# Optimization experiments

Measured on AMD Instinct MI355X. Metric: run time of the kernel, lower is better.

## Reference

```python
import jax, jax.numpy as jnp
import numpy as np

N = 50000
E = 1000000
WIDTH = 64
DEPTH = 4


def setup_inputs() -> dict:
    key = jax.random.key(0)
    ks = jax.random.split(key, 6)
    x = jax.random.normal(ks[0], (N, 5), dtype=jnp.float32)
    edge_index = jax.random.randint(ks[1], (2, E), 0, N, dtype=jnp.int32)
    edge_attr = jax.random.normal(ks[2], (E, 3), dtype=jnp.float32)
    w1 = jax.random.normal(ks[3], (3, WIDTH), dtype=jnp.float32) / jnp.sqrt(3.0)
    b1 = jnp.zeros((WIDTH,), jnp.float32)
    w2 = jax.random.normal(ks[4], (WIDTH, 1), dtype=jnp.float32) / jnp.sqrt(float(WIDTH))
    b2 = jnp.zeros((1,), jnp.float32)
    root = jax.random.normal(ks[5], (1, 1), dtype=jnp.float32)
    bias = jnp.zeros((1,), jnp.float32)
    return dict(x=x, edge_index=edge_index, edge_attr=edge_attr,
                w1=w1, b1=b1, w2=w2, b2=b2, root=root, bias=bias)


def reference(x, edge_index, edge_attr, w1, b1, w2, b2, root, bias):
    # h: scalar node feature, column 2 of data.x -> [N, 1]
    h = x[:, 2:3]
    src, dst = edge_index[0], edge_index[1]  # messages flow src -> dst

    # Per-edge 1x1 weight from the edge MLP (depends only on edge_attr,
    # identical for all depth iterations since the conv is shared).
    w_e = jax.nn.relu(edge_attr @ w1 + b1) @ w2 + b2  # [E, 1]

    # Mean aggregation: precompute in-degree of each target node.
    deg = jax.ops.segment_sum(jnp.ones((E,), jnp.float32), dst, num_segments=N)
    inv_deg = jnp.where(deg > 0, 1.0 / jnp.maximum(deg, 1.0), 0.0)[:, None]  # [N, 1]

    for _ in range(DEPTH):
        msg = h[src] * w_e                                        # gather + per-edge weight, [E, 1]
        agg = jax.ops.segment_sum(msg, dst, num_segments=N) * inv_deg  # scatter-mean, [N, 1]
        h = jax.nn.relu(agg + h @ root + bias)                    # root transform + bias + ReLU
    return h
```

## Files before the change

kernel.cpp:

```cpp
#include <hip/hip_runtime.h>

#define NN 50000
#define NNP 50176
#define NE 1000000
#define NBK 196
#define ESTRIDE 5632
#define EPB4 5120

#define EPB 1024
#define PB 977

__global__ __launch_bounds__(1024)
void place4(const float* __restrict__ x,
            const float* __restrict__ ea,
            const int* __restrict__ src,
            const int* __restrict__ dst,
            const float* __restrict__ w1,
            const float* __restrict__ b1,
            const float* __restrict__ w2,
            const float* __restrict__ b2,
            uint2* __restrict__ es,
            int* __restrict__ ebase,
            float* __restrict__ hA) {
    __shared__ float sw1[192];
    __shared__ float sb1[64];
    __shared__ float sw2[64];
    __shared__ int hist[NBK];
    __shared__ int part[256];
    __shared__ int lexcl[NBK];
    __shared__ uint2 eLDS[EPB4];
    const int t = threadIdx.x;
    const int j = blockIdx.x;
    if (t < 192) sw1[t] = w1[t];
    if (t < 64) { sb1[t] = b1[t]; sw2[t] = w2[t]; }
    if (t < NBK) hist[t] = 0;
    {
        int i = j * 1024 + t;
        if (i < NN) hA[i] = x[5 * i + 2];
    }
    __syncthreads();
    const float bz = b2[0];
    const int e0 = j * EPB4;
    const int myN = (NE - e0 < EPB4) ? (NE - e0) : EPB4;

    float ce[5];
    int dd[5], rr[5], ss[5];
#pragma unroll
    for (int k = 0; k < 5; ++k) {
        int p = k * 1024 + t;
        dd[k] = -1;
        if (p < myN) {
            int e = e0 + p;
            float a0 = ea[3 * e + 0];
            float a1 = ea[3 * e + 1];
            float a2 = ea[3 * e + 2];
            float c0 = bz, c1 = 0.f, c2 = 0.f, c3 = 0.f;
#pragma unroll
            for (int kk = 0; kk < 64; kk += 4) {
                float h0 = fmaf(a0, sw1[kk+0], fmaf(a1, sw1[64+kk+0], fmaf(a2, sw1[128+kk+0], sb1[kk+0])));
                float h1 = fmaf(a0, sw1[kk+1], fmaf(a1, sw1[64+kk+1], fmaf(a2, sw1[128+kk+1], sb1[kk+1])));
                float h2 = fmaf(a0, sw1[kk+2], fmaf(a1, sw1[64+kk+2], fmaf(a2, sw1[128+kk+2], sb1[kk+2])));
                float h3 = fmaf(a0, sw1[kk+3], fmaf(a1, sw1[64+kk+3], fmaf(a2, sw1[128+kk+3], sb1[kk+3])));
                c0 = fmaf(fmaxf(h0, 0.f), sw2[kk+0], c0);
                c1 = fmaf(fmaxf(h1, 0.f), sw2[kk+1], c1);
                c2 = fmaf(fmaxf(h2, 0.f), sw2[kk+2], c2);
                c3 = fmaf(fmaxf(h3, 0.f), sw2[kk+3], c3);
            }
            ce[k] = (c0 + c1) + (c2 + c3);
            ss[k] = src[e];
            int d = dst[e];
            dd[k] = d;
            rr[k] = atomicAdd(&hist[d >> 8], 1);
        }
    }
    __syncthreads();
    int val = 0;
    if (t < 256) { val = (t < NBK) ? hist[t] : 0; part[t] = val; }
    __syncthreads();
    for (int off = 1; off < 256; off <<= 1) {
        int xv = 0, add = 0;
        if (t < 256) { xv = part[t]; if (t >= off) add = part[t - off]; }
        __syncthreads();
        if (t < 256) part[t] = xv + add;
        __syncthreads();
    }
    if (t < NBK) {
        int excl = part[t] - val;
        lexcl[t] = excl;
        ebase[j * NBK + t] = (excl << 16) | val;
    }
    __syncthreads();
#pragma unroll
    for (int k = 0; k < 5; ++k) {
        if (dd[k] >= 0) {
            int d = dd[k];
            int pos = lexcl[d >> 8] + rr[k];
            eLDS[pos] = make_uint2((unsigned)ss[k] | ((unsigned)(d & 255) << 17),
                                   __float_as_uint(ce[k]));
        }
    }
    __syncthreads();
    for (int p = t; p < myN; p += 1024)
        es[e0 + p] = eLDS[p];
}

__global__ __launch_bounds__(1024)
void sortround1(const int* __restrict__ ebase,
                const uint2* __restrict__ es,
                uint2* __restrict__ es2,
                uint2* __restrict__ nodePtr,
                const float* __restrict__ hold,
                float* __restrict__ hnew,
                const float* __restrict__ root,
                const float* __restrict__ bias) {
    __shared__ int cbase[NBK + 1];
    __shared__ int cex[NBK];
    __shared__ int hist[256];
    __shared__ int part[256];
    __shared__ int cur[256];
    __shared__ float lagg[256];
    const int t = threadIdx.x;
    const int b = blockIdx.x;
    if (t < 256) { hist[t] = 0; lagg[t] = 0.f; }
    int c = 0;
    if (t < NBK) {
        int pk = ebase[t * NBK + b];
        cex[t] = pk >> 16;
        c = pk & 0xFFFF;
    }
    if (t < 256) part[t] = (t < NBK) ? c : 0;
    __syncthreads();
    for (int off = 1; off < 256; off <<= 1) {
        int xv = 0, add = 0;
        if (t < 256) { xv = part[t]; if (t >= off) add = part[t - off]; }
        __syncthreads();
        if (t < 256) part[t] = xv + add;
        __syncthreads();
    }
    if (t < NBK) cbase[t] = part[t] - c;
    if (t == 0) cbase[NBK] = part[NBK - 1];
    __syncthreads();
    const int C = cbase[NBK];

    uint2 v[6]; int key[6]; bool m[6];
#pragma unroll
    for (int k = 0; k < 6; ++k) {
        int p = k * 1024 + t;
        m[k] = (p < C);
        if (m[k]) {
            int lo = 0, hi = NBK - 1;
            while (lo < hi) { int mid = (lo + hi + 1) >> 1; if (cbase[mid] <= p) lo = mid; else hi = mid - 1; }
            v[k] = es[lo * EPB4 + cex[lo] + (p - cbase[lo])];
            key[k] = (v[k].x >> 17) & 255;
            atomicAdd(&hist[key[k]], 1);
        }
    }
    __syncthreads();
    int val = 0;
    if (t < 256) { val = hist[t]; part[t] = val; }
    __syncthreads();
    for (int off = 1; off < 256; off <<= 1) {
        int xv = 0, add = 0;
        if (t < 256) { xv = part[t]; if (t >= off) add = part[t - off]; }
        __syncthreads();
        if (t < 256) part[t] = xv + add;
        __syncthreads();
    }
    if (t < 256) {
        int excl = part[t] - val;
        cur[t] = excl;
        int ec = (excl < ESTRIDE) ? excl : ESTRIDE;
        nodePtr[b * 256 + t] = make_uint2((unsigned)(b * ESTRIDE + ec), (unsigned)val);
    }
    __syncthreads();
#pragma unroll
    for (int k = 0; k < 6; ++k) {
        if (m[k]) {
            int pos = atomicAdd(&cur[key[k]], 1);
            if (pos < ESTRIDE) es2[b * ESTRIDE + pos] = v[k];
            atomicAdd(&lagg[key[k]], hold[v[k].x & 0x1FFFF] * __uint_as_float(v[k].y));
        }
    }
    __syncthreads();
    if (t < 256) {
        int node = b * 256 + t;
        if (node < NN) {
            float inv = (val > 0) ? (1.0f / (float)val) : 0.f;
            hnew[node] = fmaxf(fmaf(hold[node], root[0], fmaf(lagg[t], inv, bias[0])), 0.f);
        }
    }
}

__global__ __launch_bounds__(256)
void round_csr(const uint2* __restrict__ nodePtr,
               const uint2* __restrict__ es2,
               const float* __restrict__ hold,
               float* __restrict__ hnew,
               const float* __restrict__ root,
               const float* __restrict__ bias) {
    int g = blockIdx.x * 256 + threadIdx.x;
    int row = g >> 3;
    int sub = g & 7;
    uint2 pk = nodePtr[row];
    int beg = (int)pk.x;
    int len = (int)pk.y;
    float acc = 0.f;
    for (int k = sub; k < len; k += 8) {
        uint2 v = es2[beg + k];
        acc += hold[v.x & 0x1FFFF] * __uint_as_float(v.y);
    }
    acc += __shfl_xor(acc, 1);
    acc += __shfl_xor(acc, 2);
    acc += __shfl_xor(acc, 4);
    if (sub == 0 && row < NN) {
        float inv = (len > 0) ? (1.0f / (float)len) : 0.f;
        hnew[row] = fmaxf(fmaf(hold[row], root[0], fmaf(acc, inv, bias[0])), 0.f);
    }
}

__global__ void bucket_count(const int* __restrict__ dst, int* __restrict__ bcnt,
                             const float* __restrict__ x, float* __restrict__ h) {
    __shared__ int hist[NBK];
    int t = threadIdx.x;
    if (t < NBK) hist[t] = 0;
    __syncthreads();
    int gid = blockIdx.x * 256 + t;
    if (gid < NN) h[gid] = x[5 * gid + 2];
#pragma unroll
    for (int j = 0; j < 4; ++j) {
        int e = blockIdx.x * EPB + j * 256 + t;
        if (e < NE) atomicAdd(&hist[dst[e] >> 8], 1);
    }
    __syncthreads();
    if (t < NBK && hist[t]) atomicAdd(&bcnt[t], hist[t]);
}

__global__ void bucket_scan(const int* __restrict__ bcnt,
                            int* __restrict__ sBeg,
                            int* __restrict__ cursor,
                            int* __restrict__ sLim) {
    __shared__ int part[256];
    int t = threadIdx.x;
    int v = (t < NBK) ? ((bcnt[t] + 1) & ~1) : 0;
    part[t] = v;
    __syncthreads();
    for (int off = 1; off < 256; off <<= 1) {
        int x = part[t];
        int add = (t >= off) ? part[t - off] : 0;
        __syncthreads();
        part[t] = x + add;
        __syncthreads();
    }
    if (t < NBK) {
        int excl = part[t] - v;
        sBeg[t] = excl;
        cursor[t] = excl;
        sLim[t] = 0x7FFFFFFF;
    }
}

__global__ void place_kernel(const float* __restrict__ ea,
                             const int* __restrict__ src,
                             const int* __restrict__ dst,
                             const float* __restrict__ w1,
                             const float* __restrict__ b1,
                             const float* __restrict__ w2,
                             const float* __restrict__ b2,
                             const int* __restrict__ sLim,
                             int* __restrict__ cursor,
                             uint2* __restrict__ es,
                             int dumpbase) {
    __shared__ float sw1[192];
    __shared__ float sb1[64];
    __shared__ float sw2[64];
    __shared__ float sce[EPB];
    __shared__ int hist[NBK];
    __shared__ int hbase[NBK];
    int t = threadIdx.x;
    if (t < 192) sw1[t] = w1[t];
    if (t < 64) { sb1[t] = b1[t]; sw2[t] = w2[t]; }
    if (t < NBK) hist[t] = 0;
    __syncthreads();

    int r[4], dd[4];
#pragma unroll
    for (int j = 0; j < 4; ++j) {
        int e = blockIdx.x * EPB + j * 256 + t;
        dd[j] = -1;
        if (e < NE) {
            float a0 = ea[3 * e + 0];
            float a1 = ea[3 * e + 1];
            float a2 = ea[3 * e + 2];
            float c0 = b2[0], c1 = 0.f, c2 = 0.f, c3 = 0.f;
#pragma unroll
            for (int k = 0; k < 64; k += 4) {
                float h0 = fmaf(a0, sw1[k+0], fmaf(a1, sw1[64+k+0], fmaf(a2, sw1[128+k+0], sb1[k+0])));
                float h1 = fmaf(a0, sw1[k+1], fmaf(a1, sw1[64+k+1], fmaf(a2, sw1[128+k+1], sb1[k+1])));
                float h2 = fmaf(a0, sw1[k+2], fmaf(a1, sw1[64+k+2], fmaf(a2, sw1[128+k+2], sb1[k+2])));
                float h3 = fmaf(a0, sw1[k+3], fmaf(a1, sw1[64+k+3], fmaf(a2, sw1[128+k+3], sb1[k+3])));
                c0 = fmaf(fmaxf(h0, 0.f), sw2[k+0], c0);
                c1 = fmaf(fmaxf(h1, 0.f), sw2[k+1], c1);
                c2 = fmaf(fmaxf(h2, 0.f), sw2[k+2], c2);
                c3 = fmaf(fmaxf(h3, 0.f), sw2[k+3], c3);
            }
            sce[j * 256 + t] = (c0 + c1) + (c2 + c3);
            int d = dst[e];
            dd[j] = d;
            r[j] = atomicAdd(&hist[d >> 8], 1);
        }
    }
    __syncthreads();
    if (t < NBK) { int hv = hist[t]; if (hv) hbase[t] = atomicAdd(&cursor[t], hv); }
    __syncthreads();
#pragma unroll
    for (int j = 0; j < 4; ++j) {
        int e = blockIdx.x * EPB + j * 256 + t;
        if (e < NE) {
            int d = dd[j];
            int b = d >> 8;
            int pos = hbase[b] + r[j];
            if (pos >= sLim[b]) pos = dumpbase + (t & 63);
            unsigned pack = (unsigned)src[e] | ((unsigned)(d & 255) << 17);
            es[pos] = make_uint2(pack, __float_as_uint(sce[j * 256 + t]));
        }
    }
}

template<int FIRST>
__global__ __launch_bounds__(1024)
void round_fused_fb(const int* __restrict__ sBeg,
                    const int* __restrict__ sEnd,
                    const int* __restrict__ sLim,
                    const uint2* __restrict__ es,
                    const float* __restrict__ hold,
                    float* __restrict__ hnew,
                    float* __restrict__ invdeg,
                    const float* __restrict__ root,
                    const float* __restrict__ bias) {
    __shared__ float lagg[256];
    __shared__ int ldeg[256];
    int t = threadIdx.x;
    int b = blockIdx.x;
    if (t < 256) { lagg[t] = 0.f; if (FIRST) ldeg[t] = 0; }
    __syncthreads();
    int s0 = sBeg[b];
    int s1 = sEnd[b];
    { int cap = sLim[b]; if (s1 > cap) s1 = cap; }
    const uint4* es4 = (const uint4*)es;
    for (int p = s0 + t * 2; p < s1; p += 2048) {
        uint4 v = es4[p >> 1];
        {
            int sidx = v.x & 0x1FFFF;
            int dl = (v.x >> 17) & 255;
            atomicAdd(&lagg[dl], hold[sidx] * __uint_as_float(v.y));
            if (FIRST) atomicAdd(&ldeg[dl], 1);
        }
        if (p + 1 < s1) {
            int sidx = v.z & 0x1FFFF;
            int dl = (v.z >> 17) & 255;
            atomicAdd(&lagg[dl], hold[sidx] * __uint_as_float(v.w));
            if (FIRST) atomicAdd(&ldeg[dl], 1);
        }
    }
    __syncthreads();
    if (t < 256) {
        int node = b * 256 + t;
        if (node < NN) {
            float inv;
            if (FIRST) {
                int d = ldeg[t];
                inv = (d > 0) ? (1.0f / (float)d) : 0.f;
                invdeg[node] = inv;
            } else {
                inv = invdeg[node];
            }
            hnew[node] = fmaxf(fmaf(hold[node], root[0], fmaf(lagg[t], inv, bias[0])), 0.f);
        }
    }
}


extern "C" void kernel_launch(void* const* d_in, const int* in_sizes, int n_in,
                              void* d_out, int out_size, void* d_ws, size_t ws_size,
                              hipStream_t stream) {
    const float* x    = (const float*)d_in[0];
    const int*   ei   = (const int*)d_in[1];
    const float* ea   = (const float*)d_in[2];
    const float* w1   = (const float*)d_in[3];
    const float* b1   = (const float*)d_in[4];
    const float* w2   = (const float*)d_in[5];
    const float* b2   = (const float*)d_in[6];
    const float* root = (const float*)d_in[7];
    const float* bias = (const float*)d_in[8];

    const int* src = ei;
    const int* dst = ei + NE;
    float* out = (float*)d_out;

    const size_t esN  = (size_t)NBK * EPB4;
    const size_t es2N = (size_t)NBK * ESTRIDE + 64;
    const size_t needFixed = esN * 8 + es2N * 8
                           + (size_t)(NBK * NBK) * 4
                           + (size_t)NNP * 8
                           + (size_t)NN * 4 * 2;

    if (ws_size >= needFixed) {
        uint2* es      = (uint2*)d_ws;
        uint2* es2     = es + esN;
        int*   ebase   = (int*)(es2 + es2N);
        uint2* nodePtr = (uint2*)(ebase + NBK * NBK);
        float* hA      = (float*)(nodePtr + NNP);
        float* hB      = hA + NN;

        place4<<<NBK, 1024, 0, stream>>>(x, ea, src, dst, w1, b1, w2, b2,
                                         es, ebase, hA);
        sortround1<<<NBK, 1024, 0, stream>>>(ebase, es, es2, nodePtr,
                                             hA, hB, root, bias);
        const int gR = NNP * 8 / 256;
        round_csr<<<gR, 256, 0, stream>>>(nodePtr, es2, hB, hA, root, bias);
        round_csr<<<gR, 256, 0, stream>>>(nodePtr, es2, hA, hB, root, bias);
        round_csr<<<gR, 256, 0, stream>>>(nodePtr, es2, hB, out, root, bias);
    } else {
        uint2* es     = (uint2*)d_ws;
        int*   bcnt   = (int*)(es + NE + NBK);
        int*   cursor = bcnt + NBK;
        int*   sBeg   = cursor + NBK;
        int*   sLim   = sBeg + NBK;
        float* invdeg = (float*)(sLim + NBK);
        float* hB     = invdeg + NN;
        float* h      = out;

        hipMemsetAsync(bcnt, 0, NBK * 4, stream);
        bucket_count<<<PB, 256, 0, stream>>>(dst, bcnt, x, h);
        bucket_scan<<<1, 256, 0, stream>>>(bcnt, sBeg, cursor, sLim);
        place_kernel<<<PB, 256, 0, stream>>>(ea, src, dst, w1, b1, w2, b2,
                                             sLim, cursor, es, 0);
        round_fused_fb<1><<<NBK, 1024, 0, stream>>>(sBeg, cursor, sLim, es, h,  hB, invdeg, root, bias);
        round_fused_fb<0><<<NBK, 1024, 0, stream>>>(sBeg, cursor, sLim, es, hB, h,  invdeg, root, bias);
        round_fused_fb<0><<<NBK, 1024, 0, stream>>>(sBeg, cursor, sLim, es, h,  hB, invdeg, root, bias);
        round_fused_fb<0><<<NBK, 1024, 0, stream>>>(sBeg, cursor, sLim, es, hB, h,  invdeg, root, bias);
    }
}
```

Measured before the change: 138.4 us.

## Vectorize edge loads in place4 with 4 edges per thread over 245 chunks

Result: slower. 179.0 us (+29.4%).

```diff
diff --git a/kernel.cpp b/kernel.cpp
--- a/kernel.cpp
+++ b/kernel.cpp
@@ -5,7 +5,8 @@
 #define NE 1000000
 #define NBK 196
 #define ESTRIDE 5632
-#define EPB4 5120
+#define EPC 4096
+#define NCH 245
 
 #define EPB 1024
 #define PB 977
@@ -28,7 +29,7 @@
     __shared__ int hist[NBK];
     __shared__ int part[256];
     __shared__ int lexcl[NBK];
-    __shared__ uint2 eLDS[EPB4];
+    __shared__ __align__(16) uint2 eLDS[EPC];
     const int t = threadIdx.x;
     const int j = blockIdx.x;
     if (t < 192) sw1[t] = w1[t];
@@ -40,37 +41,50 @@
     }
     __syncthreads();
     const float bz = b2[0];
-    const int e0 = j * EPB4;
-    const int myN = (NE - e0 < EPB4) ? (NE - e0) : EPB4;
-
-    float ce[5];
-    int dd[5], rr[5], ss[5];
-#pragma unroll
-    for (int k = 0; k < 5; ++k) {
-        int p = k * 1024 + t;
-        dd[k] = -1;
-        if (p < myN) {
-            int e = e0 + p;
-            float a0 = ea[3 * e + 0];
-            float a1 = ea[3 * e + 1];
-            float a2 = ea[3 * e + 2];
-            float c0 = bz, c1 = 0.f, c2 = 0.f, c3 = 0.f;
-#pragma unroll
-            for (int kk = 0; kk < 64; kk += 4) {
-                float h0 = fmaf(a0, sw1[kk+0], fmaf(a1, sw1[64+kk+0], fmaf(a2, sw1[128+kk+0], sb1[kk+0])));
-                float h1 = fmaf(a0, sw1[kk+1], fmaf(a1, sw1[64+kk+1], fmaf(a2, sw1[128+kk+1], sb1[kk+1])));
-                float h2 = fmaf(a0, sw1[kk+2], fmaf(a1, sw1[64+kk+2], fmaf(a2, sw1[128+kk+2], sb1[kk+2])));
-                float h3 = fmaf(a0, sw1[kk+3], fmaf(a1, sw1[64+kk+3], fmaf(a2, sw1[128+kk+3], sb1[kk+3])));
-                c0 = fmaf(fmaxf(h0, 0.f), sw2[kk+0], c0);
-                c1 = fmaf(fmaxf(h1, 0.f), sw2[kk+1], c1);
-                c2 = fmaf(fmaxf(h2, 0.f), sw2[kk+2], c2);
-                c3 = fmaf(fmaxf(h3, 0.f), sw2[kk+3], c3);
+    const int e0 = j * EPC;
+    const int myN = (NE - e0 < EPC) ? (NE - e0) : EPC;
+    const bool act = (4 * t < myN);
+
+    float4 A0, A1, A2; int4 s4, d4;
+    if (act) {
+        const float4* eav = (const float4*)(ea + 3 * (size_t)e0);
+        A0 = eav[3 * t + 0];
+        A1 = eav[3 * t + 1];
+        A2 = eav[3 * t + 2];
+        s4 = ((const int4*)(src + e0))[t];
+        d4 = ((const int4*)(dst + e0))[t];
+    }
+    float ax[4], ay[4], az[4];
+    ax[0] = A0.x; ay[0] = A0.y; az[0] = A0.z;
+    ax[1] = A0.w; ay[1] = A1.x; az[1] = A1.y;
+    ax[2] = A1.z; ay[2] = A1.w; az[2] = A2.x;
+    ax[3] = A2.y; ay[3] = A2.z; az[3] = A2.w;
+    int dd[4]; dd[0] = d4.x; dd[1] = d4.y; dd[2] = d4.z; dd[3] = d4.w;
+    int ss[4]; ss[0] = s4.x; ss[1] = s4.y; ss[2] = s4.z; ss[3] = s4.w;
+
+    float c[4][4];
+    float ce[4]; int rr[4];
+    if (act) {
+#pragma unroll
+        for (int e = 0; e < 4; ++e) { c[e][0] = bz; c[e][1] = 0.f; c[e][2] = 0.f; c[e][3] = 0.f; }
+#pragma unroll
+        for (int kk = 0; kk < 64; kk += 4) {
+#pragma unroll
+            for (int e = 0; e < 4; ++e) {
+                float h0 = fmaf(ax[e], sw1[kk+0], fmaf(ay[e], sw1[64+kk+0], fmaf(az[e], sw1[128+kk+0], sb1[kk+0])));
+                float h1 = fmaf(ax[e], sw1[kk+1], fmaf(ay[e], sw1[64+kk+1], fmaf(az[e], sw1[128+kk+1], sb1[kk+1])));
+                float h2 = fmaf(ax[e], sw1[kk+2], fmaf(ay[e], sw1[64+kk+2], fmaf(az[e], sw1[128+kk+2], sb1[kk+2])));
+                float h3 = fmaf(ax[e], sw1[kk+3], fmaf(ay[e], sw1[64+kk+3], fmaf(az[e], sw1[128+kk+3], sb1[kk+3])));
+                c[e][0] = fmaf(fmaxf(h0, 0.f), sw2[kk+0], c[e][0]);
+                c[e][1] = fmaf(fmaxf(h1, 0.f), sw2[kk+1], c[e][1]);
+                c[e][2] = fmaf(fmaxf(h2, 0.f), sw2[kk+2], c[e][2]);
+                c[e][3] = fmaf(fmaxf(h3, 0.f), sw2[kk+3], c[e][3]);
             }
-            ce[k] = (c0 + c1) + (c2 + c3);
-            ss[k] = src[e];
-            int d = dst[e];
-            dd[k] = d;
-            rr[k] = atomicAdd(&hist[d >> 8], 1);
+        }
+#pragma unroll
+        for (int e = 0; e < 4; ++e) {
+            ce[e] = (c[e][0] + c[e][1]) + (c[e][2] + c[e][3]);
+            rr[e] = atomicAdd(&hist[dd[e] >> 8], 1);
         }
     }
     __syncthreads();
@@ -90,18 +104,21 @@
         ebase[j * NBK + t] = (excl << 16) | val;
     }
     __syncthreads();
-#pragma unroll
-    for (int k = 0; k < 5; ++k) {
-        if (dd[k] >= 0) {
-            int d = dd[k];
-            int pos = lexcl[d >> 8] + rr[k];
-            eLDS[pos] = make_uint2((unsigned)ss[k] | ((unsigned)(d & 255) << 17),
-                                   __float_as_uint(ce[k]));
-        }
-    }
-    __syncthreads();
-    for (int p = t; p < myN; p += 1024)
-        es[e0 + p] = eLDS[p];
+    if (act) {
+#pragma unroll
+        for (int e = 0; e < 4; ++e) {
+            int d = dd[e];
+            int pos = lexcl[d >> 8] + rr[e];
+            eLDS[pos] = make_uint2((unsigned)ss[e] | ((unsigned)(d & 255) << 17),
+                                   __float_as_uint(ce[e]));
+        }
+    }
+    __syncthreads();
+    {
+        uint4* dst4 = (uint4*)(es + e0);
+        const uint4* src4l = (const uint4*)eLDS;
+        for (int i = t; i < (myN >> 1); i += 1024) dst4[i] = src4l[i];
+    }
 }
 
 __global__ __launch_bounds__(1024)
@@ -113,8 +130,8 @@
                 float* __restrict__ hnew,
                 const float* __restrict__ root,
                 const float* __restrict__ bias) {
-    __shared__ int cbase[NBK + 1];
-    __shared__ int cex[NBK];
+    __shared__ int cbase[NCH + 1];
+    __shared__ int cex[NCH];
     __shared__ int hist[256];
     __shared__ int part[256];
     __shared__ int cur[256];
@@ -123,12 +140,12 @@
     const int b = blockIdx.x;
     if (t < 256) { hist[t] = 0; lagg[t] = 0.f; }
     int c = 0;
-    if (t < NBK) {
+    if (t < NCH) {
         int pk = ebase[t * NBK + b];
         cex[t] = pk >> 16;
         c = pk & 0xFFFF;
     }
-    if (t < 256) part[t] = (t < NBK) ? c : 0;
+    if (t < 256) part[t] = (t < NCH) ? c : 0;
     __syncthreads();
     for (int off = 1; off < 256; off <<= 1) {
         int xv = 0, add = 0;
@@ -137,10 +154,10 @@
         if (t < 256) part[t] = xv + add;
         __syncthreads();
     }
-    if (t < NBK) cbase[t] = part[t] - c;
-    if (t == 0) cbase[NBK] = part[NBK - 1];
-    __syncthreads();
-    const int C = cbase[NBK];
+    if (t < NCH) cbase[t] = part[t] - c;
+    if (t == 0) cbase[NCH] = part[NCH - 1];
+    __syncthreads();
+    const int C = cbase[NCH];
 
     uint2 v[6]; int key[6]; bool m[6];
 #pragma unroll
@@ -148,9 +165,9 @@
         int p = k * 1024 + t;
         m[k] = (p < C);
         if (m[k]) {
-            int lo = 0, hi = NBK - 1;
+            int lo = 0, hi = NCH - 1;
             while (lo < hi) { int mid = (lo + hi + 1) >> 1; if (cbase[mid] <= p) lo = mid; else hi = mid - 1; }
-            v[k] = es[lo * EPB4 + cex[lo] + (p - cbase[lo])];
+            v[k] = es[lo * EPC + cex[lo] + (p - cbase[lo])];
             key[k] = (v[k].x >> 17) & 255;
             atomicAdd(&hist[key[k]], 1);
         }
@@ -397,10 +414,10 @@
     const int* dst = ei + NE;
     float* out = (float*)d_out;
 
-    const size_t esN  = (size_t)NBK * EPB4;
+    const size_t esN  = (size_t)NCH * EPC;
     const size_t es2N = (size_t)NBK * ESTRIDE + 64;
     const size_t needFixed = esN * 8 + es2N * 8
-                           + (size_t)(NBK * NBK) * 4
+                           + (size_t)(NCH * NBK) * 4
                            + (size_t)NNP * 8
                            + (size_t)NN * 4 * 2;
 
@@ -408,11 +425,11 @@
         uint2* es      = (uint2*)d_ws;
         uint2* es2     = es + esN;
         int*   ebase   = (int*)(es2 + es2N);
-        uint2* nodePtr = (uint2*)(ebase + NBK * NBK);
+        uint2* nodePtr = (uint2*)(ebase + NCH * NBK);
         float* hA      = (float*)(nodePtr + NNP);
         float* hB      = hA + NN;
 
-        place4<<<NBK, 1024, 0, stream>>>(x, ea, src, dst, w1, b1, w2, b2,
+        place4<<<NCH, 1024, 0, stream>>>(x, ea, src, dst, w1, b1, w2, b2,
                                          es, ebase, hA);
         sortround1<<<NBK, 1024, 0, stream>>>(ebase, es, es2, nodePtr,
                                              hA, hB, root, bias);
```
